# Performance work log

Measured on AMD Instinct MI355X. Metric: run time of the kernel, lower is better.

The kernel has to match this reference:

```python
import jax, jax.numpy as jnp
import numpy as np

B, NB, BS, K = 16, 512, 128, 32
N = NB * BS
GRAPH_WEIGHT = 0.3


def setup_inputs() -> dict:
    key = jax.random.key(0)
    k1, k2, k3, k4, k5 = jax.random.split(key, 5)
    logits = jax.random.normal(k1, (B, N, 1), dtype=jnp.float32)
    targets = jax.random.bernoulli(k2, 0.5, (B, N)).astype(jnp.float32)[..., None]
    r = jax.random.uniform(k3, (B, N))
    sup_mask = r < 0.10
    ignore_mask = (r >= 0.10) & (r < 0.20)
    kv_indices = jax.random.randint(k4, (B, NB, K), 0, NB).astype(jnp.int32)
    kv_num_blocks = jax.random.randint(k5, (B, NB), 0, K + 1).astype(jnp.int32)
    return {
        "logits": logits,
        "targets": targets,
        "sup_mask": sup_mask,
        "ignore_mask": ignore_mask,
        "kv_indices": kv_indices,
        "kv_num_blocks": kv_num_blocks,
        "block_size": BS,
    }


def _bce_masked_mean(x, t, m):
    # numerically stable BCE-with-logits, mean over masked entries
    per = jnp.maximum(x, 0.0) - x * t + jnp.log1p(jnp.exp(-jnp.abs(x)))
    mf = m.astype(x.dtype)
    cnt = mf.sum()
    return (per * mf).sum() / jnp.maximum(cnt, 1.0)


def _graph_smoothness(logits, sup_mask, ignore_mask, kv_indices, kv_num_blocks, block_size):
    b, n = sup_mask.shape
    nb = n // block_size
    probs = jax.nn.sigmoid(logits[..., 0])                 # [B, N]
    pb = probs.reshape(b, nb, block_size)                  # [B, NB, BS]
    unc = (~ignore_mask & ~sup_mask).reshape(b, nb, block_size)  # uncertain q nodes
    vld = (~ignore_mask).reshape(b, nb, block_size)        # valid neighbor nodes

    bidx = jnp.arange(b)[:, None, None]
    neigh_p = pb[bidx, kv_indices]                         # [B, NB, K, BS]
    neigh_v = vld[bidx, kv_indices]                        # [B, NB, K, BS]
    k = kv_indices.shape[-1]
    slot_ok = jnp.arange(k)[None, None, :] < kv_num_blocks[:, :, None]  # [B, NB, K]
    nmask = (neigh_v & slot_ok[..., None]).astype(probs.dtype)          # [B, NB, K, BS]

    cnt = nmask.sum(axis=(-1, -2))                         # [B, NB] neighbor counts
    nmean = (neigh_p * nmask).sum(axis=(-1, -2)) / jnp.maximum(cnt, 1.0)

    q_unc_cnt = unc.sum(axis=-1)                           # [B, NB]
    block_ok = (q_unc_cnt > 0) & (kv_num_blocks > 0) & (cnt > 0)
    sq = (((pb - nmean[..., None]) ** 2) * unc.astype(probs.dtype)).sum(-1)  # [B, NB]
    loss_b = jnp.where(block_ok, sq, 0.0).sum(-1)          # [B]
    n_unc_b = jnp.where(block_ok, q_unc_cnt, 0).sum(-1).astype(probs.dtype)  # [B]
    batch_ok = n_unc_b > 0
    per_batch = jnp.where(batch_ok, loss_b / jnp.maximum(n_unc_b, 1.0), 0.0)
    n_valid = batch_ok.sum().astype(probs.dtype)
    return per_batch.sum() / jnp.maximum(n_valid, 1.0)


def reference(logits, targets, sup_mask, ignore_mask, kv_indices, kv_num_blocks, block_size):
    loss_sup = _bce_masked_mean(logits[..., 0], targets[..., 0], sup_mask)
    loss_graph = _graph_smoothness(logits, sup_mask, ignore_mask,
                                   kv_indices, kv_num_blocks, block_size)
    return loss_sup + GRAPH_WEIGHT * loss_graph
```

## Files before the change

kernel.cpp:

```cpp
#include <hip/hip_runtime.h>
#include <math.h>

#define BB 16
#define NBB 512
#define BSS 128
#define KK 32
#define NBLK (BB*NBB)
#define STATS_GRID 1024


__global__ __launch_bounds__(256) void stats_kernel(
    const float* __restrict__ logits, const float* __restrict__ targets,
    const unsigned char* __restrict__ sup_b, const unsigned char* __restrict__ ign_b,
    float* __restrict__ W)
{
    const int t = threadIdx.x;
    __shared__ int s_mode;
    if (t == 0) s_mode = 0;
    __syncthreads();
    int local = 0;
    #pragma unroll
    for (int r = 0; r < 4; ++r) {
        if (sup_b[4 * (t + 256 * r) + 1] != 0) local = 1;
    }
    if (local) atomicOr(&s_mode, 1);
    __syncthreads();
    const bool byteMode = (s_mode != 0);

    const int gid = blockIdx.x * 256 + t;
    const float4 x4 = ((const float4*)logits)[gid];
    const float4 t4 = ((const float4*)targets)[gid];
    bool s[4], g[4];
    if (byteMode) {
        const unsigned int sm = ((const unsigned int*)sup_b)[gid];
        const unsigned int gm = ((const unsigned int*)ign_b)[gid];
        #pragma unroll
        for (int j = 0; j < 4; ++j) {
            s[j] = ((sm >> (8 * j)) & 0xffu) != 0;
            g[j] = ((gm >> (8 * j)) & 0xffu) != 0;
        }
    } else {
        const int4 sm = ((const int4*)sup_b)[gid];
        const int4 gm = ((const int4*)ign_b)[gid];
        s[0] = sm.x != 0; s[1] = sm.y != 0; s[2] = sm.z != 0; s[3] = sm.w != 0;
        g[0] = gm.x != 0; g[1] = gm.y != 0; g[2] = gm.z != 0; g[3] = gm.w != 0;
    }
    const float xs[4] = {x4.x, x4.y, x4.z, x4.w};
    const float ts[4] = {t4.x, t4.y, t4.z, t4.w};

    float svp = 0.f, cv = 0.f, su = 0.f, su2 = 0.f, cu = 0.f, bs = 0.f, bc = 0.f;
    #pragma unroll
    for (int j = 0; j < 4; ++j) {
        const float x = xs[j];
        const float p = 1.0f / (1.0f + expf(-x));
        if (s[j]) {
            bs += fmaxf(x, 0.0f) - x * ts[j] + log1pf(expf(-fabsf(x)));
            bc += 1.0f;
        }
        if (!g[j]) {
            svp += p; cv += 1.0f;
            if (!s[j]) { su += p; su2 += p * p; cu += 1.0f; }
        }
    }
    #pragma unroll
    for (int off = 16; off > 0; off >>= 1) {
        svp += __shfl_down(svp, off, 32);
        cv  += __shfl_down(cv,  off, 32);
        su  += __shfl_down(su,  off, 32);
        su2 += __shfl_down(su2, off, 32);
        cu  += __shfl_down(cu,  off, 32);
        bs  += __shfl_down(bs,  off, 32);
        bc  += __shfl_down(bc,  off, 32);
    }
    if ((t & 31) == 0) {
        const int qb = blockIdx.x * 8 + (t >> 5);
        W[qb]           = svp;
        W[8192  + qb]   = cv;
        W[16384 + qb]   = su;
        W[24576 + qb]   = su2;
        W[32768 + qb]   = cu;
        W[40960 + qb]   = bs;
        W[49152 + qb]   = bc;
    }
    if (blockIdx.x == 0 && t == 0) {
        #pragma unroll
        for (int i = 0; i < 34; ++i) W[57344 + i] = 0.0f;
        *((int*)(W + 57384)) = 0;
    }
}

__global__ __launch_bounds__(64) void graph_kernel(
    const int* __restrict__ kv_idx, const int* __restrict__ kv_nb,
    float* __restrict__ W, float* __restrict__ out)
{
    const int t  = threadIdx.x;
    const int b  = blockIdx.x >> 3;
    const int i  = ((blockIdx.x & 7) << 6) + t;
    const int gb = b * NBB + i;

    const float* Svp  = W;
    const float* Cv   = W + 8192;
    const float* Sup  = W + 16384;
    const float* Sup2 = W + 24576;
    const float* Cu   = W + 32768;
    const float* bceS = W + 40960;
    const float* bceC = W + 49152;
    float* P     = W + 57344;
    int* ticket  = (int*)(W + 57384);

    float bs = bceS[gb];
    float bc = bceC[gb];
    const int knb = kv_nb[gb];
    const int* idx = kv_idx + (size_t)gb * KK;
    float cnt = 0.f, psum = 0.f;
    for (int k = 0; k < knb; ++k) {
        const int j = idx[k];
        cnt  += Cv[b * NBB + j];
        psum += Svp[b * NBB + j];
    }
    const float cu = Cu[gb];
    float loss = 0.f, nunc = 0.f;
    if (cu > 0.0f && knb > 0 && cnt > 0.0f) {
        const float m = psum / fmaxf(cnt, 1.0f);
        loss = Sup2[gb] - 2.0f * m * Sup[gb] + m * m * cu;
        nunc = cu;
    }
    #pragma unroll
    for (int off = 32; off > 0; off >>= 1) {
        loss += __shfl_down(loss, off);
        nunc += __shfl_down(nunc, off);
        bs   += __shfl_down(bs,   off);
        bc   += __shfl_down(bc,   off);
    }
    if (t == 0) {
        atomicAdd(&P[b * 2 + 0], loss);
        atomicAdd(&P[b * 2 + 1], nunc);
        atomicAdd(&P[32], bs);
        atomicAdd(&P[33], bc);
        __threadfence();
        const int rank = atomicAdd(ticket, 1);
        if (rank == 127) {
            __threadfence();
            float gsum = 0.f, nval = 0.f;
            for (int b2 = 0; b2 < BB; ++b2) {
                const float l = atomicAdd(&P[b2 * 2 + 0], 0.0f);
                const float n = atomicAdd(&P[b2 * 2 + 1], 0.0f);
                if (n > 0.0f) { gsum += l / fmaxf(n, 1.0f); nval += 1.0f; }
            }
            const float tbs = atomicAdd(&P[32], 0.0f);
            const float tbc = atomicAdd(&P[33], 0.0f);
            out[0] = tbs / fmaxf(tbc, 1.0f) + 0.3f * (gsum / fmaxf(nval, 1.0f));
        }
    }
}

extern "C" void kernel_launch(void* const* d_in, const int* in_sizes, int n_in,
                              void* d_out, int out_size, void* d_ws, size_t ws_size,
                              hipStream_t stream) {
    (void)in_sizes; (void)n_in; (void)out_size; (void)ws_size;
    const float* logits  = (const float*)d_in[0];
    const float* targets = (const float*)d_in[1];
    const unsigned char* supm = (const unsigned char*)d_in[2];
    const unsigned char* ignm = (const unsigned char*)d_in[3];
    const int* kv_idx = (const int*)d_in[4];
    const int* kv_nb  = (const int*)d_in[5];
    float* W   = (float*)d_ws;
    float* out = (float*)d_out;

    hipLaunchKernelGGL(stats_kernel, dim3(STATS_GRID), dim3(256), 0, stream,
                       logits, targets, supm, ignm, W);
    hipLaunchKernelGGL(graph_kernel, dim3(128), dim3(64), 0, stream,
                       kv_idx, kv_nb, W, out);
}
```

Baseline: 103.0 us.

## Parallelize neighbor gather across 32-lane groups and pack per-block stats

The graph kernel now assigns each query block to a 32-lane group, so each lane loads one neighbor index and its stats, and shuffles reduce the results. Before, one thread looped serially over up to 32 neighbors. Per-block statistics are packed into float2/float4 records so each gather or read is a single vector load. The grid grows to 256 blocks of 256 threads, with a shared-memory reduction before the atomics. This removes the long serial dependent-load chain in the latency-bound second kernel.

```diff
diff --git a/kernel.cpp b/kernel.cpp
--- a/kernel.cpp
+++ b/kernel.cpp
@@ -8,6 +8,12 @@
 #define NBLK (BB*NBB)
 #define STATS_GRID 1024
 
+
+#define VC_OFF 0
+#define SU_OFF 16384
+#define BC_OFF 49152
+#define P_OFF  65536
+#define TICKET_OFF 65570
 
 __global__ __launch_bounds__(256) void stats_kernel(
     const float* __restrict__ logits, const float* __restrict__ targets,
@@ -74,78 +80,86 @@
     }
     if ((t & 31) == 0) {
         const int qb = blockIdx.x * 8 + (t >> 5);
-        W[qb]           = svp;
-        W[8192  + qb]   = cv;
-        W[16384 + qb]   = su;
-        W[24576 + qb]   = su2;
-        W[32768 + qb]   = cu;
-        W[40960 + qb]   = bs;
-        W[49152 + qb]   = bc;
+        ((float2*)(W + VC_OFF))[qb] = make_float2(svp, cv);
+        ((float4*)(W + SU_OFF))[qb] = make_float4(su, su2, cu, 0.0f);
+        ((float2*)(W + BC_OFF))[qb] = make_float2(bs, bc);
     }
     if (blockIdx.x == 0 && t == 0) {
         #pragma unroll
-        for (int i = 0; i < 34; ++i) W[57344 + i] = 0.0f;
-        *((int*)(W + 57384)) = 0;
+        for (int i = 0; i < 34; ++i) W[P_OFF + i] = 0.0f;
+        *((int*)(W + TICKET_OFF)) = 0;
     }
 }
 
-__global__ __launch_bounds__(64) void graph_kernel(
+__global__ __launch_bounds__(256) void graph_kernel(
     const int* __restrict__ kv_idx, const int* __restrict__ kv_nb,
     float* __restrict__ W, float* __restrict__ out)
 {
-    const int t  = threadIdx.x;
-    const int b  = blockIdx.x >> 3;
-    const int i  = ((blockIdx.x & 7) << 6) + t;
-    const int gb = b * NBB + i;
+    const int t    = threadIdx.x;
+    const int grp  = t >> 5;
+    const int slot = t & 31;
+    const int b    = blockIdx.x >> 4;
 
-    const float* Svp  = W;
-    const float* Cv   = W + 8192;
-    const float* Sup  = W + 16384;
-    const float* Sup2 = W + 24576;
-    const float* Cu   = W + 32768;
-    const float* bceS = W + 40960;
-    const float* bceC = W + 49152;
-    float* P     = W + 57344;
-    int* ticket  = (int*)(W + 57384);
+    const float2* __restrict__ VC  = (const float2*)(W + VC_OFF);
+    const float4* __restrict__ SU  = (const float4*)(W + SU_OFF);
+    const float2* __restrict__ BCp = (const float2*)(W + BC_OFF);
+    float* P    = W + P_OFF;
+    int* ticket = (int*)(W + TICKET_OFF);
+    const float2* __restrict__ VCb = VC + (b << 9);
 
-    float bs = bceS[gb];
-    float bc = bceC[gb];
-    const int knb = kv_nb[gb];
-    const int* idx = kv_idx + (size_t)gb * KK;
-    float cnt = 0.f, psum = 0.f;
-    for (int k = 0; k < knb; ++k) {
-        const int j = idx[k];
-        cnt  += Cv[b * NBB + j];
-        psum += Svp[b * NBB + j];
+    float loss_a = 0.f, nunc_a = 0.f, bs_a = 0.f, bc_a = 0.f;
+    #pragma unroll
+    for (int qq = 0; qq < 4; ++qq) {
+        const int gb  = blockIdx.x * 32 + grp * 4 + qq;
+        const int knb = kv_nb[gb];
+        float psum = 0.f, cnt = 0.f;
+        if (slot < knb) {
+            const int j = kv_idx[(size_t)gb * KK + slot];
+            const float2 vc = VCb[j];
+            psum = vc.x; cnt = vc.y;
+        }
+        #pragma unroll
+        for (int m = 16; m > 0; m >>= 1) {
+            psum += __shfl_xor(psum, m, 32);
+            cnt  += __shfl_xor(cnt,  m, 32);
+        }
+        if (slot == 0) {
+            const float4 su  = SU[gb];
+            const float2 bcv = BCp[gb];
+            bs_a += bcv.x; bc_a += bcv.y;
+            if (su.z > 0.0f && knb > 0 && cnt > 0.0f) {
+                const float mm = psum / fmaxf(cnt, 1.0f);
+                loss_a += su.y - 2.0f * mm * su.x + mm * mm * su.z;
+                nunc_a += su.z;
+            }
+        }
     }
-    const float cu = Cu[gb];
-    float loss = 0.f, nunc = 0.f;
-    if (cu > 0.0f && knb > 0 && cnt > 0.0f) {
-        const float m = psum / fmaxf(cnt, 1.0f);
-        loss = Sup2[gb] - 2.0f * m * Sup[gb] + m * m * cu;
-        nunc = cu;
+
+    __shared__ float s[8][4];
+    if (slot == 0) {
+        s[grp][0] = loss_a; s[grp][1] = nunc_a;
+        s[grp][2] = bs_a;   s[grp][3] = bc_a;
     }
-    #pragma unroll
-    for (int off = 32; off > 0; off >>= 1) {
-        loss += __shfl_down(loss, off);
-        nunc += __shfl_down(nunc, off);
-        bs   += __shfl_down(bs,   off);
-        bc   += __shfl_down(bc,   off);
-    }
+    __syncthreads();
     if (t == 0) {
-        atomicAdd(&P[b * 2 + 0], loss);
-        atomicAdd(&P[b * 2 + 1], nunc);
+        float l = 0.f, n = 0.f, bs = 0.f, bc = 0.f;
+        #pragma unroll
+        for (int g = 0; g < 8; ++g) {
+            l += s[g][0]; n += s[g][1]; bs += s[g][2]; bc += s[g][3];
+        }
+        atomicAdd(&P[b * 2 + 0], l);
+        atomicAdd(&P[b * 2 + 1], n);
         atomicAdd(&P[32], bs);
         atomicAdd(&P[33], bc);
         __threadfence();
         const int rank = atomicAdd(ticket, 1);
-        if (rank == 127) {
+        if (rank == 255) {
             __threadfence();
             float gsum = 0.f, nval = 0.f;
             for (int b2 = 0; b2 < BB; ++b2) {
-                const float l = atomicAdd(&P[b2 * 2 + 0], 0.0f);
-                const float n = atomicAdd(&P[b2 * 2 + 1], 0.0f);
-                if (n > 0.0f) { gsum += l / fmaxf(n, 1.0f); nval += 1.0f; }
+                const float lv = atomicAdd(&P[b2 * 2 + 0], 0.0f);
+                const float nv = atomicAdd(&P[b2 * 2 + 1], 0.0f);
+                if (nv > 0.0f) { gsum += lv / fmaxf(nv, 1.0f); nval += 1.0f; }
             }
             const float tbs = atomicAdd(&P[32], 0.0f);
             const float tbc = atomicAdd(&P[33], 0.0f);
@@ -169,6 +183,6 @@
 
     hipLaunchKernelGGL(stats_kernel, dim3(STATS_GRID), dim3(256), 0, stream,
                        logits, targets, supm, ignm, W);
-    hipLaunchKernelGGL(graph_kernel, dim3(128), dim3(64), 0, stream,
+    hipLaunchKernelGGL(graph_kernel, dim3(256), dim3(256), 0, stream,
                        kv_idx, kv_nb, W, out);
 }
```

After: 106.9 us. +3.8%, slower.
